# Kernel tuning notes

Hardware: AMD Instinct MI355X
Metric: run time of the kernel (lower is better)

Reference implementation:

```python
import jax, jax.numpy as jnp
import numpy as np

B, S, HID = 2, 2048, 1024
H, HKV, D = 16, 8, 128
G = H // HKV
EPS = 1e-6
ROPE_BASE = 1e6


def _rms_norm(x, w):
    # per-last-dim RMSNorm in fp32, matching QwenRMSNorm
    x32 = x.astype(jnp.float32)
    var = jnp.mean(x32 * x32, axis=-1, keepdims=True)
    return w * (x32 * jax.lax.rsqrt(var + EPS)).astype(x.dtype)


def _rotate_half(x):
    half = x.shape[-1] // 2
    return jnp.concatenate([-x[..., half:], x[..., :half]], axis=-1)


def setup_inputs() -> dict:
    key = jax.random.key(0)
    ks = jax.random.split(key, 6)
    return {
        "hidden_states": jax.random.normal(ks[0], (B, S, HID), dtype=jnp.float32),
        "position_ids": jnp.arange(S, dtype=jnp.int32),
        "Wq": jax.random.normal(ks[1], (HID, H * D), dtype=jnp.float32) * 0.02,
        "Wk": jax.random.normal(ks[2], (HID, HKV * D), dtype=jnp.float32) * 0.02,
        "Wv": jax.random.normal(ks[3], (HID, HKV * D), dtype=jnp.float32) * 0.02,
        "Wo": jax.random.normal(ks[4], (H * D, HID), dtype=jnp.float32) * 0.02,
        "q_norm_w": jnp.ones((D,), dtype=jnp.float32),
        "k_norm_w": jnp.ones((D,), dtype=jnp.float32),
    }


def reference(hidden_states, position_ids, Wq, Wk, Wv, Wo, q_norm_w, k_norm_w):
    b, s, _ = hidden_states.shape
    # projections
    q = (hidden_states @ Wq).reshape(b, s, H, D)
    k = (hidden_states @ Wk).reshape(b, s, HKV, D)
    v = (hidden_states @ Wv).reshape(b, s, HKV, D)
    # QK RMSNorm (per head_dim), then [B, heads, S, D]
    q = _rms_norm(q, q_norm_w).transpose(0, 2, 1, 3)
    k = _rms_norm(k, k_norm_w).transpose(0, 2, 1, 3)
    v = v.transpose(0, 2, 1, 3)
    # RoPE
    inv_freq = 1.0 / (ROPE_BASE ** (jnp.arange(0, D, 2, dtype=jnp.float32) / D))
    freqs = position_ids.astype(jnp.float32)[:, None] * inv_freq[None, :]  # [S, D/2]
    emb = jnp.concatenate([freqs, freqs], axis=-1)  # [S, D]
    cos = jnp.cos(emb)[None, None, :, :].astype(q.dtype)
    sin = jnp.sin(emb)[None, None, :, :].astype(q.dtype)
    q = q * cos + _rotate_half(q) * sin
    k = k * cos + _rotate_half(k) * sin
    # GQA attention without materializing repeated K/V:
    # q heads h = kh*G + g  <->  repeat_interleave(G, dim=1) of kv heads
    qg = q.reshape(b, HKV, G, s, D)
    scale = 1.0 / jnp.sqrt(jnp.asarray(D, dtype=q.dtype))
    scores = jnp.einsum('bhgqd,bhkd->bhgqk', qg, k) * scale  # [B,HKV,G,S,S]
    causal = jnp.tril(jnp.ones((s, s), dtype=bool))
    scores = jnp.where(causal[None, None, None, :, :], scores, jnp.finfo(scores.dtype).min)
    probs = jax.nn.softmax(scores, axis=-1)
    attn = jnp.einsum('bhgqk,bhkd->bhgqd', probs, v)  # [B,HKV,G,S,D]
    attn = attn.reshape(b, H, s, D).transpose(0, 2, 1, 3).reshape(b, s, H * D)
    out = attn @ Wo
    return out, k, v
```

## Files before the change

### kernel.cpp

```cpp
#include <hip/hip_runtime.h>

#define B_ 2
#define S_ 2048
#define HID_ 1024
#define H_ 16
#define HKV_ 8
#define D_ 128

typedef unsigned short u16;
typedef __attribute__((ext_vector_type(8))) short short8;
typedef __attribute__((ext_vector_type(4))) float f32x4;
typedef __attribute__((ext_vector_type(16))) float f32x16;
typedef __attribute__((ext_vector_type(2))) unsigned short u16x2;
typedef __attribute__((ext_vector_type(4))) unsigned short u16x4;
typedef const __attribute__((address_space(1))) void gvoid;
typedef __attribute__((address_space(3))) void svoid;

__device__ __forceinline__ u16 f2b(float f) {
  union { float f; unsigned u; } v; v.f = f;
  unsigned r = v.u + 0x7FFFu + ((v.u >> 16) & 1u);
  return (u16)(r >> 16);
}
__device__ __forceinline__ float b2f(u16 x) {
  union { unsigned u; float f; } v; v.u = ((unsigned)x) << 16; return v.f;
}

__device__ __forceinline__ float exp2_fast(float x) {
  float r; asm("v_exp_f32 %0, %1" : "=v"(r) : "v"(x)); return r;
}
__device__ __forceinline__ unsigned cvtpk_bf16(float lo, float hi) {
  unsigned r; asm("v_cvt_pk_bf16_f32 %0, %1, %2" : "=v"(r) : "v"(lo), "v"(hi)); return r;
}
__device__ __forceinline__ void vm_drain() {
  asm volatile("s_waitcnt vmcnt(0)" ::: "memory");
  __builtin_amdgcn_sched_barrier(0);
}
__device__ __forceinline__ int swz8(int r) {
  return (r & 3) | ((((r >> 2) ^ (r >> 3)) & 1) << 2);
}

__device__ __forceinline__ void transpose_dev(const float* __restrict__ W,
                                              u16* __restrict__ Wt,
                                              int K, int N, bool PERM, int bid,
                                              float (*t)[33]) {
  const int nb = N >> 5;
  const int bx = bid % nb;
  const int by = bid / nb;
  const int tx = threadIdx.x & 31, ty = threadIdx.x >> 5;
#pragma unroll
  for (int i = 0; i < 32; i += 8)
    t[ty + i][tx] = W[(size_t)(by * 32 + ty + i) * N + bx * 32 + tx];
  __syncthreads();
#pragma unroll
  for (int i = 0; i < 32; i += 8) {
    int n = bx * 32 + ty + i;
    int nn;
    if (PERM) {
      int head = n >> 7, d = n & 127;
      int p = (d & 15) | (((d >> 6) & 1) << 4) | (((d >> 4) & 1) << 5) | (((d >> 5) & 1) << 6);
      nn = head * 128 + p;
    } else {
      nn = n;
    }
    Wt[(size_t)nn * K + by * 32 + tx] = f2b(t[tx][ty + i]);
  }
}

__global__ __launch_bounds__(256) void prep_kernel(const float* __restrict__ hs,
                                                   u16* __restrict__ Xb,
                                                   const float* __restrict__ Wq,
                                                   const float* __restrict__ Wk,
                                                   const float* __restrict__ Wv,
                                                   const float* __restrict__ Wo,
                                                   u16* __restrict__ Wqkvt,
                                                   u16* __restrict__ Wot,
                                                   const int* __restrict__ pid,
                                                   float* __restrict__ ct,
                                                   float* __restrict__ st) {
  __shared__ float t[32][33];
  const int bid = blockIdx.x;
  if (bid < 4096) {
    int i = bid * 256 + threadIdx.x;
    const float4 v = ((const float4*)hs)[i];
    u16x4 o = { f2b(v.x), f2b(v.y), f2b(v.z), f2b(v.w) };
    ((u16x4*)Xb)[i] = o;
  } else if (bid < 6144) {
    transpose_dev(Wq, Wqkvt, 1024, 2048, true, bid - 4096, t);
  } else if (bid < 7168) {
    transpose_dev(Wk, Wqkvt + (size_t)2048 * 1024, 1024, 1024, true, bid - 6144, t);
  } else if (bid < 8192) {
    transpose_dev(Wv, Wqkvt + (size_t)3072 * 1024, 1024, 1024, false, bid - 7168, t);
  } else if (bid < 10240) {
    transpose_dev(Wo, Wot, 2048, 1024, false, bid - 8192, t);
  } else {
    int i = (bid - 10240) * 256 + threadIdx.x;
    int f = i >> 11, s = i & 2047;
    double inv = exp2(-(double)f * (19.931568569324174 / 64.0));
    double ang = (double)pid[s] * inv;
    ct[i] = (float)cos(ang);
    st[i] = (float)sin(ang);
  }
}

template <int M, int N, int K, int BM>
__global__ __launch_bounds__(256) void gemm_bt(const u16* __restrict__ A,
                                               const u16* __restrict__ Bt,
                                               float* __restrict__ C) {
  __shared__ u16 As[BM * 64];
  __shared__ u16 Bs[128 * 64];
  const int tid = threadIdx.x;
  const int w = tid >> 6;
  const int l = tid & 63;
  const int l15 = l & 15, lg = l >> 4;
  const int nbx = N / 128;
  const int bx = blockIdx.x % nbx, by = blockIdx.x / nbx;
  const int row0 = by * BM, col0 = bx * 128;
  const int wr = w >> 1, wc = w & 1;
  constexpr int MR = BM / 32;

  f32x4 acc[MR][4];
#pragma unroll
  for (int m = 0; m < MR; ++m)
#pragma unroll
    for (int n = 0; n < 4; ++n) acc[m][n] = (f32x4){0.f, 0.f, 0.f, 0.f};

  for (int k0 = 0; k0 < K; k0 += 64) {
    __syncthreads();
#pragma unroll
    for (int i = 0; i < BM / 32; ++i) {
      int c = i * 256 + tid;
      int r = c >> 3, cc = c & 7;
      int cs = cc ^ swz8(r);
      const u16* sa = A + (size_t)(row0 + r) * K + k0 + cs * 8;
      __builtin_amdgcn_global_load_lds((gvoid*)sa, (svoid*)(As + (i * 256 + w * 64) * 8), 16, 0, 0);
    }
#pragma unroll
    for (int i = 0; i < 4; ++i) {
      int c = i * 256 + tid;
      int r = c >> 3, cc = c & 7;
      int cs = cc ^ swz8(r);
      const u16* sb = Bt + (size_t)(col0 + r) * K + k0 + cs * 8;
      __builtin_amdgcn_global_load_lds((gvoid*)sb, (svoid*)(Bs + (i * 256 + w * 64) * 8), 16, 0, 0);
    }
    vm_drain();
    __syncthreads();
#pragma unroll
    for (int kk = 0; kk < 2; ++kk) {
      short8 af[MR], bf[4];
#pragma unroll
      for (int m = 0; m < MR; ++m) {
        const int row = wr * (BM / 2) + m * 16 + l15;
        af[m] = *(const short8*)((const char*)As + row * 128 +
                                 (((kk * 4 + lg) ^ swz8(row)) << 4));
      }
#pragma unroll
      for (int n = 0; n < 4; ++n) {
        const int row = wc * 64 + n * 16 + l15;
        bf[n] = *(const short8*)((const char*)Bs + row * 128 +
                                 (((kk * 4 + lg) ^ swz8(row)) << 4));
      }
#pragma unroll
      for (int m = 0; m < MR; ++m)
#pragma unroll
        for (int n = 0; n < 4; ++n)
          acc[m][n] = __builtin_amdgcn_mfma_f32_16x16x32_bf16(af[m], bf[n], acc[m][n], 0, 0, 0);
    }
  }
#pragma unroll
  for (int m = 0; m < MR; ++m)
#pragma unroll
    for (int n = 0; n < 4; ++n) {
      float* cp = C + (size_t)(row0 + wr * (BM / 2) + m * 16 + lg * 4) * N + col0 + wc * 64 + n * 16 + l15;
#pragma unroll
      for (int r = 0; r < 4; ++r) cp[(size_t)r * N] = acc[m][n][r];
    }
}

__global__ __launch_bounds__(256) void gemm_qkv_fused(const u16* __restrict__ A,
                                                      const u16* __restrict__ Bt,
                                                      const float* __restrict__ qnw,
                                                      const float* __restrict__ knw,
                                                      const float* __restrict__ ct_t,
                                                      const float* __restrict__ st_t,
                                                      u16* __restrict__ Qbb,
                                                      u16* __restrict__ Kbb,
                                                      float* __restrict__ kout,
                                                      float* __restrict__ vout,
                                                      u16* __restrict__ VTb) {
  constexpr int K = 1024;
  __shared__ u16 As[64 * 64];
  __shared__ u16 Bs[128 * 64];
  __shared__ float red[64][2];
  const int tid = threadIdx.x;
  const int w = tid >> 6;
  const int l = tid & 63;
  const int l15 = l & 15, lg = l >> 4;
  const int bx = blockIdx.x & 31, by = blockIdx.x >> 5;
  const int row0 = by * 64, col0 = bx * 128;
  const int wr = w >> 1, wc = w & 1;

  f32x4 acc[2][4];
#pragma unroll
  for (int m = 0; m < 2; ++m)
#pragma unroll
    for (int n = 0; n < 4; ++n) acc[m][n] = (f32x4){0.f, 0.f, 0.f, 0.f};

  for (int k0 = 0; k0 < K; k0 += 64) {
    __syncthreads();
#pragma unroll
    for (int i = 0; i < 2; ++i) {
      int c = i * 256 + tid;
      int r = c >> 3, cc = c & 7;
      int cs = cc ^ swz8(r);
      const u16* sa = A + (size_t)(row0 + r) * K + k0 + cs * 8;
      __builtin_amdgcn_global_load_lds((gvoid*)sa, (svoid*)(As + (i * 256 + w * 64) * 8), 16, 0, 0);
    }
#pragma unroll
    for (int i = 0; i < 4; ++i) {
      int c = i * 256 + tid;
      int r = c >> 3, cc = c & 7;
      int cs = cc ^ swz8(r);
      const u16* sb = Bt + (size_t)(col0 + r) * K + k0 + cs * 8;
      __builtin_amdgcn_global_load_lds((gvoid*)sb, (svoid*)(Bs + (i * 256 + w * 64) * 8), 16, 0, 0);
    }
    vm_drain();
    __syncthreads();
#pragma unroll
    for (int kk = 0; kk < 2; ++kk) {
      short8 af[2], bf[4];
#pragma unroll
      for (int m = 0; m < 2; ++m) {
        const int row = wr * 32 + m * 16 + l15;
        af[m] = *(const short8*)((const char*)As + row * 128 +
                                 (((kk * 4 + lg) ^ swz8(row)) << 4));
      }
#pragma unroll
      for (int n = 0; n < 4; ++n) {
        const int row = wc * 64 + n * 16 + l15;
        bf[n] = *(const short8*)((const char*)Bs + row * 128 +
                                 (((kk * 4 + lg) ^ swz8(row)) << 4));
      }
#pragma unroll
      for (int m = 0; m < 2; ++m)
#pragma unroll
        for (int n = 0; n < 4; ++n)
          acc[m][n] = __builtin_amdgcn_mfma_f32_16x16x32_bf16(af[m], bf[n], acc[m][n], 0, 0, 0);
    }
  }

  const int b_ = row0 >> 11;
  const int s0 = row0 & 2047;
  if (bx < 24) {
    float part[2][4];
#pragma unroll
    for (int m = 0; m < 2; ++m)
#pragma unroll
      for (int r = 0; r < 4; ++r) {
        float p = 0.f;
#pragma unroll
        for (int n = 0; n < 4; ++n) p += acc[m][n][r] * acc[m][n][r];
        part[m][r] = p;
      }
#pragma unroll
    for (int i = 1; i < 16; i <<= 1)
#pragma unroll
      for (int m = 0; m < 2; ++m)
#pragma unroll
        for (int r = 0; r < 4; ++r) part[m][r] += __shfl_xor(part[m][r], i, 64);
    if (l15 == 0) {
#pragma unroll
      for (int m = 0; m < 2; ++m)
#pragma unroll
        for (int r = 0; r < 4; ++r) red[wr * 32 + m * 16 + lg * 4 + r][wc] = part[m][r];
    }
    __syncthreads();

    const bool isQ = bx < 16;
    const int h = isQ ? bx : bx - 16;
    const float* nw = isQ ? qnw : knw;
    u16* outb = isQ ? Qbb : Kbb;
    const int NH = isQ ? 16 : 8;
    const float qsc = isQ ? 0.12751740027f : 1.0f;
#pragma unroll
    for (int np = 0; np < 2; ++np) {
      const int d_lo = l15 + 32 * wc + 16 * np;
      const float w_lo = nw[d_lo], w_hi = nw[d_lo + 64];
#pragma unroll
      for (int m = 0; m < 2; ++m) {
        const int sb = s0 + wr * 32 + m * 16 + lg * 4;
        const float4 cv = *(const float4*)(ct_t + d_lo * 2048 + sb);
        const float4 sv = *(const float4*)(st_t + d_lo * 2048 + sb);
#pragma unroll
        for (int r = 0; r < 4; ++r) {
          const int ro = wr * 32 + m * 16 + lg * 4 + r;
          const float tot = red[ro][0] + red[ro][1];
          const float rms = rsqrtf(tot * (1.0f / 128.0f) + 1e-6f);
          const float xl = acc[m][2 * np][r] * rms * w_lo;
          const float xh = acc[m][2 * np + 1][r] * rms * w_hi;
          const float cc = ((const float*)&cv)[r], ss = ((const float*)&sv)[r];
          const float ol = xl * cc - xh * ss;
          const float oh = xh * cc + xl * ss;
          const size_t base = ((size_t)(b_ * NH + h) * 2048 + sb + r) * 128;
          outb[base + d_lo] = f2b(ol * qsc);
          outb[base + d_lo + 64] = f2b(oh * qsc);
          if (!isQ) {
            kout[base + d_lo] = ol;
            kout[base + d_lo + 64] = oh;
          }
        }
      }
    }
  } else {
    const int h = bx - 24;
#pragma unroll
    for (int n = 0; n < 4; ++n) {
      const int d = wc * 64 + n * 16 + l15;
#pragma unroll
      for (int m = 0; m < 2; ++m) {
        const int sb = s0 + wr * 32 + m * 16 + lg * 4;
        u16x4 pk;
#pragma unroll
        for (int r = 0; r < 4; ++r) {
          const float x = acc[m][n][r];
          vout[((size_t)(b_ * 8 + h) * 2048 + sb + r) * 128 + d] = x;
          pk[r] = f2b(x);
        }
        *(u16x4*)(VTb + ((size_t)(b_ * 8 + h) * 128 + d) * 2048 + sb) = pk;
      }
    }
  }
}

__global__ __launch_bounds__(256, 3) void attn_kernel(const u16* __restrict__ Qb,
                                                      const u16* __restrict__ Kb,
                                                      const u16* __restrict__ VTb,
                                                      u16* __restrict__ Ab,
                                                      u16* __restrict__ Op,
                                                      float* __restrict__ Ml) {
  __shared__ u16 lds[2][8192];
  const int tid = threadIdx.x;
  const int w = tid >> 6, l = tid & 63;
  const int l31 = l & 31, hi = l >> 5;
  const int bid = blockIdx.x;
  const int half = bid & 1;
  const int pid = bid >> 1;
  const int b = pid >> 7;
  const int hh = (pid >> 3) & 15;
  const int p8 = pid & 7;
  const int hkv = hh >> 1;

  const u16* Kh = Kb + (size_t)(b * HKV_ + hkv) * S_ * 128;
  const u16* VTh = VTb + (size_t)(b * HKV_ + hkv) * 128 * S_;
  int cur = 0;
  const float M0 = 18.0f;

  auto stage = [&](int kt, int buf) {
    const u16* Kp = Kh + (size_t)kt * 32 * 128;
    const u16* Vp = VTh + kt * 32;
    u16* Kd = &lds[buf][0];
    u16* Vd = &lds[buf][4096];
#pragma unroll
    for (int i = 0; i < 2; ++i) {
      int c = i * 256 + tid;
      int kr = c >> 4, kc = c & 15;
      int kcs = kc ^ ((kr ^ (kr >> 3)) & 15);
      __builtin_amdgcn_global_load_lds((gvoid*)(Kp + kr * 128 + kcs * 8),
                                       (svoid*)(Kd + (i * 256 + w * 64) * 8), 16, 0, 0);
      int vd = c >> 2, vc = c & 3;
      int vcs = vc ^ ((vd >> 1) & 3);
      __builtin_amdgcn_global_load_lds((gvoid*)(Vp + (size_t)vd * S_ + vcs * 8),
                                       (svoid*)(Vd + (i * 256 + w * 64) * 8), 16, 0, 0);
    }
  };

  auto run_seg = [&](int pp, int kt0, int kt1, int mode) {
    const int q0 = pp * 128;
    const int ntp = 4 * (pp + 1);
    const int qrow = q0 + w * 32 + l31;

    short8 qf[8];
    {
      const u16* qp = Qb + ((size_t)(b * H_ + hh) * S_ + qrow) * 128 + hi * 8;
#pragma unroll
      for (int c = 0; c < 8; ++c) qf[c] = *(const short8*)(qp + c * 16);
    }

    float l_run = 0.f;
    f32x16 oacc[4];
#pragma unroll
    for (int n = 0; n < 4; ++n)
#pragma unroll
      for (int r = 0; r < 16; ++r) oacc[n][r] = 0.f;

    stage(kt0, cur);
    vm_drain();
    __syncthreads();
    for (int kt = kt0; kt < kt1; ++kt) {
      if (kt + 1 < kt1) stage(kt + 1, cur ^ 1);
      const u16* Kl = &lds[cur][0];
      const u16* Vl = &lds[cur][4096];
      const bool domask = (kt >= ntp - 4);

      f32x16 stv;
#pragma unroll
      for (int r = 0; r < 16; ++r) stv[r] = 0.f;
      {
        const int row = l31;
        const int rb = row * 256, sw = ((row ^ (row >> 3)) & 15) << 4;
        __builtin_amdgcn_s_setprio(1);
#pragma unroll
        for (int c = 0; c < 8; ++c) {
          short8 kf = *(const short8*)((const char*)Kl + rb + ((c * 32 + hi * 16) ^ sw));
          stv = __builtin_amdgcn_mfma_f32_32x32x16_bf16(kf, qf[c], stv, 0, 0, 0);
        }
        __builtin_amdgcn_s_setprio(0);
      }

#pragma unroll
      for (int h2 = 0; h2 < 2; ++h2) {
        float pv8[8];
#pragma unroll
        for (int j = 0; j < 8; ++j) {
          const int r = h2 * 8 + j;
          float x = stv[r] - M0;
          if (domask) {
            int kv = kt * 32 + (r & 3) + 8 * (r >> 2) + 4 * hi;
            if (kv > qrow) x = -1e30f;
          }
          pv8[j] = exp2_fast(x);
        }
        {
          float s0 = pv8[0] + pv8[4], s1 = pv8[1] + pv8[5];
          float s2 = pv8[2] + pv8[6], s3 = pv8[3] + pv8[7];
          l_run += (s0 + s1) + (s2 + s3);
        }
        unsigned Wl[2][2], Wx[2][2];
#pragma unroll
        for (int g = 0; g < 2; ++g)
#pragma unroll
          for (int i = 0; i < 2; ++i) {
            Wl[g][i] = cvtpk_bf16(pv8[4 * g + 2 * i], pv8[4 * g + 2 * i + 1]);
            Wx[g][i] = __shfl_xor(Wl[g][i], 32, 64);
          }
        short8 paf;
        ((unsigned*)&paf)[0] = hi ? Wx[1][0] : Wl[0][0];
        ((unsigned*)&paf)[1] = hi ? Wx[1][1] : Wl[0][1];
        ((unsigned*)&paf)[2] = hi ? Wl[1][0] : Wx[0][0];
        ((unsigned*)&paf)[3] = hi ? Wl[1][1] : Wx[0][1];
        __builtin_amdgcn_s_setprio(1);
#pragma unroll
        for (int n = 0; n < 4; ++n) {
          const int d = n * 32 + l31;
          const int ch = ((h2 * 2 + hi) ^ ((d >> 1) & 3)) << 4;
          short8 vf = *(const short8*)((const char*)Vl + d * 64 + ch);
          oacc[n] = __builtin_amdgcn_mfma_f32_32x32x16_bf16(paf, vf, oacc[n], 0, 0, 0);
        }
        __builtin_amdgcn_s_setprio(0);
      }
      vm_drain();
      __syncthreads();
      cur ^= 1;
    }

    l_run += __shfl_xor(l_run, 32, 64);

    if (mode == 0) {
#pragma unroll
      for (int r = 0; r < 16; ++r) {
        const int ql = (r & 3) + 8 * (r >> 2) + 4 * hi;
        float lb = __shfl(l_run, ql, 64);
        float inv = 1.0f / lb;
        const int q = q0 + w * 32 + ql;
        u16* op = Ab + ((size_t)(b * S_) + q) * 2048 + hh * 128 + l31;
#pragma unroll
        for (int n = 0; n < 4; ++n) op[n * 32] = f2b(oacc[n][r] * inv);
      }
    } else {
      const int part = mode - 1;
      u16* ob = Op + ((size_t)(part * 256 + pid)) * 128 * 128;
#pragma unroll
      for (int r = 0; r < 16; ++r) {
        const int ql = (r & 3) + 8 * (r >> 2) + 4 * hi;
        const int qq = w * 32 + ql;
#pragma unroll
        for (int n = 0; n < 4; ++n) ob[qq * 128 + n * 32 + l31] = f2b(oacc[n][r]);
      }
      if (hi == 0) {
        float* mlb = Ml + ((size_t)(part * 256 + pid)) * 256;
        mlb[w * 32 + l31] = l_run;
      }
    }
  };

  if (half == 0) {
    run_seg(p8, 0, 4 * p8 + 4, 0);
    run_seg(15 - p8, 0, 30 - 4 * p8, 1);
  } else {
    run_seg(15 - p8, 30 - 4 * p8, 64 - 4 * p8, 2);
  }
}

__global__ __launch_bounds__(256) void attn_combine_kernel(const u16* __restrict__ Op,
                                                           const float* __restrict__ Ml,
                                                           u16* __restrict__ Ab) {
  const int pid = blockIdx.x;
  const int b = pid >> 7, hh = (pid >> 3) & 15, p8 = pid & 7;
  const int pp = 15 - p8;
  const int q = threadIdx.x >> 1;
  const int d0 = (threadIdx.x & 1) * 64;
  const float l0 = Ml[(size_t)pid * 256 + q];
  const float l1 = Ml[(size_t)(256 + pid) * 256 + q];
  const float linv = 1.0f / (l0 + l1);
  const u16* o0 = Op + ((size_t)pid * 128 + q) * 128 + d0;
  const u16* o1 = Op + ((size_t)(256 + pid) * 128 + q) * 128 + d0;
  u16* ab = Ab + ((size_t)(b * S_) + pp * 128 + q) * 2048 + hh * 128 + d0;
#pragma unroll
  for (int c = 0; c < 8; ++c) {
    short8 a = *(const short8*)(o0 + c * 8);
    short8 bb = *(const short8*)(o1 + c * 8);
    short8 o;
#pragma unroll
    for (int j = 0; j < 8; ++j)
      o[j] = (short)f2b((b2f((u16)a[j]) + b2f((u16)bb[j])) * linv);
    *(short8*)(ab + c * 8) = o;
  }
}

extern "C" void kernel_launch(void* const* d_in, const int* in_sizes, int n_in,
                              void* d_out, int out_size, void* d_ws, size_t ws_size,
                              hipStream_t stream) {
  const float* hs  = (const float*)d_in[0];
  const int*   pid = (const int*)d_in[1];
  const float* Wq  = (const float*)d_in[2];
  const float* Wk  = (const float*)d_in[3];
  const float* Wv  = (const float*)d_in[4];
  const float* Wo  = (const float*)d_in[5];
  const float* qnw = (const float*)d_in[6];
  const float* knw = (const float*)d_in[7];

  float* out0 = (float*)d_out;
  float* kout = out0 + (size_t)B_ * HKV_ * S_ * D_;
  float* vout = kout + (size_t)B_ * HKV_ * S_ * D_;

  char* ws = (char*)d_ws;
  size_t off = 0;
  auto alloc = [&](size_t bytes) {
    void* p = ws + off;
    off += (bytes + 255) & ~(size_t)255;
    return p;
  };
  u16*   Xb    = (u16*)alloc((size_t)4096 * 1024 * 2);
  u16*   Wqkvt = (u16*)alloc((size_t)4096 * 1024 * 2);
  u16*   Wot   = (u16*)alloc((size_t)1024 * 2048 * 2);
  float* ct_t  = (float*)alloc((size_t)64 * 2048 * 4);
  float* st_t  = (float*)alloc((size_t)64 * 2048 * 4);
  u16*   Qbb   = (u16*)alloc((size_t)B_ * H_ * S_ * D_ * 2);
  u16*   Kbb   = (u16*)alloc((size_t)B_ * HKV_ * S_ * D_ * 2);
  u16*   VTb   = (u16*)alloc((size_t)B_ * HKV_ * D_ * S_ * 2);
  u16*   Ab    = (u16*)alloc((size_t)B_ * S_ * H_ * D_ * 2);
  u16*   Op    = (u16*)alloc((size_t)2 * 256 * 128 * 128 * 2);
  float* Ml    = (float*)alloc((size_t)2 * 256 * 256 * 4);

  prep_kernel<<<10752, 256, 0, stream>>>(hs, Xb, Wq, Wk, Wv, Wo, Wqkvt, Wot,
                                         pid, ct_t, st_t);

  gemm_qkv_fused<<<2048, 256, 0, stream>>>(Xb, Wqkvt, qnw, knw, ct_t, st_t,
                                           Qbb, Kbb, kout, vout, VTb);

  attn_kernel<<<512, 256, 0, stream>>>(Qbb, Kbb, VTb, Ab, Op, Ml);
  attn_combine_kernel<<<256, 256, 0, stream>>>(Op, Ml, Ab);

  gemm_bt<4096, 1024, 2048, 64><<<8 * 64, 256, 0, stream>>>(Ab, Wot, out0);
}
```

Measured before the change: 161.1 us.

## Split causal attention work into three balanced segments per query-tile pair

```diff
diff --git a/kernel.cpp b/kernel.cpp
--- a/kernel.cpp
+++ b/kernel.cpp
@@ -342,8 +342,8 @@
   const int w = tid >> 6, l = tid & 63;
   const int l31 = l & 31, hi = l >> 5;
   const int bid = blockIdx.x;
-  const int half = bid & 1;
-  const int pid = bid >> 1;
+  const int sid = bid >> 8;
+  const int pid = bid & 255;
   const int b = pid >> 7;
   const int hh = (pid >> 3) & 15;
   const int p8 = pid & 7;
@@ -464,7 +464,7 @@
 
     l_run += __shfl_xor(l_run, 32, 64);
 
-    if (mode == 0) {
+    if (mode < 0) {
 #pragma unroll
       for (int r = 0; r < 16; ++r) {
         const int ql = (r & 3) + 8 * (r >> 2) + 4 * hi;
@@ -476,8 +476,7 @@
         for (int n = 0; n < 4; ++n) op[n * 32] = f2b(oacc[n][r] * inv);
       }
     } else {
-      const int part = mode - 1;
-      u16* ob = Op + ((size_t)(part * 256 + pid)) * 128 * 128;
+      u16* ob = Op + ((size_t)(mode * 256 + pid)) * 128 * 128;
 #pragma unroll
       for (int r = 0; r < 16; ++r) {
         const int ql = (r & 3) + 8 * (r >> 2) + 4 * hi;
@@ -486,42 +485,66 @@
         for (int n = 0; n < 4; ++n) ob[qq * 128 + n * 32 + l31] = f2b(oacc[n][r]);
       }
       if (hi == 0) {
-        float* mlb = Ml + ((size_t)(part * 256 + pid)) * 256;
+        float* mlb = Ml + ((size_t)(mode * 256 + pid)) * 128;
         mlb[w * 32 + l31] = l_run;
       }
     }
   };
 
-  if (half == 0) {
-    run_seg(p8, 0, 4 * p8 + 4, 0);
-    run_seg(15 - p8, 0, 30 - 4 * p8, 1);
+  const int lenA = 4 * p8 + 4;
+  const int lenB = 64 - 4 * p8;
+  if (p8 <= 4) {
+    if (sid == 0) {
+      run_seg(p8, 0, lenA, -1);
+      run_seg(15 - p8, 0, 23 - lenA, 0);
+    } else if (sid == 1) {
+      run_seg(15 - p8, 23 - lenA, 45 - lenA, 1);
+    } else {
+      run_seg(15 - p8, 45 - lenA, lenB, 2);
+    }
   } else {
-    run_seg(15 - p8, 30 - 4 * p8, 64 - 4 * p8, 2);
+    if (sid == 0) {
+      run_seg(p8, 0, 23, 0);
+    } else if (sid == 1) {
+      run_seg(p8, 23, lenA, 1);
+      run_seg(15 - p8, 0, 45 - lenA, 2);
+    } else {
+      run_seg(15 - p8, 45 - lenA, lenB, 3);
+    }
   }
 }
 
 __global__ __launch_bounds__(256) void attn_combine_kernel(const u16* __restrict__ Op,
                                                            const float* __restrict__ Ml,
                                                            u16* __restrict__ Ab) {
-  const int pid = blockIdx.x;
-  const int b = pid >> 7, hh = (pid >> 3) & 15, p8 = pid & 7;
-  const int pp = 15 - p8;
+  const int idx = blockIdx.x;
+  const int which = idx >> 8;
+  const int pid = idx & 255;
+  const int p8 = pid & 7;
+  if (which == 1 && p8 <= 4) return;
+  const int b = pid >> 7, hh = (pid >> 3) & 15;
+  const int pp = which ? p8 : 15 - p8;
+  int ns, js[3];
+  if (which == 1)      { ns = 2; js[0] = 0; js[1] = 1; js[2] = 0; }
+  else if (p8 <= 4)    { ns = 3; js[0] = 0; js[1] = 1; js[2] = 2; }
+  else                 { ns = 2; js[0] = 2; js[1] = 3; js[2] = 0; }
   const int q = threadIdx.x >> 1;
   const int d0 = (threadIdx.x & 1) * 64;
-  const float l0 = Ml[(size_t)pid * 256 + q];
-  const float l1 = Ml[(size_t)(256 + pid) * 256 + q];
-  const float linv = 1.0f / (l0 + l1);
-  const u16* o0 = Op + ((size_t)pid * 128 + q) * 128 + d0;
-  const u16* o1 = Op + ((size_t)(256 + pid) * 128 + q) * 128 + d0;
+  float lsum = 0.f;
+  for (int i = 0; i < ns; ++i) lsum += Ml[((size_t)(js[i] * 256 + pid)) * 128 + q];
+  const float linv = 1.0f / lsum;
   u16* ab = Ab + ((size_t)(b * S_) + pp * 128 + q) * 2048 + hh * 128 + d0;
 #pragma unroll
   for (int c = 0; c < 8; ++c) {
-    short8 a = *(const short8*)(o0 + c * 8);
-    short8 bb = *(const short8*)(o1 + c * 8);
+    float a8[8] = {0.f, 0.f, 0.f, 0.f, 0.f, 0.f, 0.f, 0.f};
+    for (int i = 0; i < ns; ++i) {
+      short8 a = *(const short8*)(Op + ((size_t)(js[i] * 256 + pid) * 128 + q) * 128 + d0 + c * 8);
+#pragma unroll
+      for (int j = 0; j < 8; ++j) a8[j] += b2f((u16)a[j]);
+    }
     short8 o;
 #pragma unroll
-    for (int j = 0; j < 8; ++j)
-      o[j] = (short)f2b((b2f((u16)a[j]) + b2f((u16)bb[j])) * linv);
+    for (int j = 0; j < 8; ++j) o[j] = (short)f2b(a8[j] * linv);
     *(short8*)(ab + c * 8) = o;
   }
 }
@@ -558,8 +581,8 @@
   u16*   Kbb   = (u16*)alloc((size_t)B_ * HKV_ * S_ * D_ * 2);
   u16*   VTb   = (u16*)alloc((size_t)B_ * HKV_ * D_ * S_ * 2);
   u16*   Ab    = (u16*)alloc((size_t)B_ * S_ * H_ * D_ * 2);
-  u16*   Op    = (u16*)alloc((size_t)2 * 256 * 128 * 128 * 2);
-  float* Ml    = (float*)alloc((size_t)2 * 256 * 256 * 4);
+  u16*   Op    = (u16*)alloc((size_t)4 * 256 * 128 * 128 * 2);
+  float* Ml    = (float*)alloc((size_t)4 * 256 * 128 * 4);
 
   prep_kernel<<<10752, 256, 0, stream>>>(hs, Xb, Wq, Wk, Wv, Wo, Wqkvt, Wot,
                                          pid, ct_t, st_t);
@@ -567,8 +590,8 @@
   gemm_qkv_fused<<<2048, 256, 0, stream>>>(Xb, Wqkvt, qnw, knw, ct_t, st_t,
                                            Qbb, Kbb, kout, vout, VTb);
 
-  attn_kernel<<<512, 256, 0, stream>>>(Qbb, Kbb, VTb, Ab, Op, Ml);
-  attn_combine_kernel<<<256, 256, 0, stream>>>(Op, Ml, Ab);
+  attn_kernel<<<768, 256, 0, stream>>>(Qbb, Kbb, VTb, Ab, Op, Ml);
+  attn_combine_kernel<<<512, 256, 0, stream>>>(Op, Ml, Ab);
 
   gemm_bt<4096, 1024, 2048, 64><<<8 * 64, 256, 0, stream>>>(Ab, Wot, out0);
 }
```

Result: slower. 190.1 us (+18.0%).
